# Optimization experiments

Hardware: AMD Instinct MI355X
Metric: run time of the kernel (lower is better)

## Reference

```python
import jax, jax.numpy as jnp
import numpy as np
import math

B, S, D, H = 2, 2048, 2048, 16
HD = D // H  # 128


def _rope(x, cos, sin):
    # x: [b, s, h, hd]; cos/sin: [s, hd//2]
    # torch view_as_complex pairs adjacent elements: (even=real, odd=imag)
    xr = x[..., 0::2]
    xi = x[..., 1::2]
    c = cos[None, :, None, :]
    s = sin[None, :, None, :]
    out_r = xr * c - xi * s
    out_i = xr * s + xi * c
    # interleave back: [..., hd//2, 2] -> [..., hd]
    return jnp.stack([out_r, out_i], axis=-1).reshape(x.shape)


def setup_inputs() -> dict:
    key = jax.random.key(0)
    ks = jax.random.split(key, 5)
    x = jax.random.normal(ks[0], (B, S, D), dtype=jnp.float32)
    std = 1.0 / math.sqrt(D)
    wq = jax.random.normal(ks[1], (D, D), dtype=jnp.float32) * std
    wk = jax.random.normal(ks[2], (D, D), dtype=jnp.float32) * std
    wv = jax.random.normal(ks[3], (D, D), dtype=jnp.float32) * std
    wo = jax.random.normal(ks[4], (D, D), dtype=jnp.float32) * std
    # RoPE frequencies, theta = 10000
    freqs = 1.0 / (10000.0 ** (jnp.arange(0, HD, 2, dtype=jnp.float32) / HD))  # [hd//2]
    t = jnp.arange(S, dtype=jnp.float32)
    angles = jnp.outer(t, freqs)  # [s, hd//2]
    freqs_cos = jnp.cos(angles)
    freqs_sin = jnp.sin(angles)
    # causal additive mask [s, s]
    mask = jnp.triu(jnp.full((S, S), -jnp.inf, dtype=jnp.float32), k=1)
    return {"x": x, "start_pos": 0, "freqs_cos": freqs_cos, "freqs_sin": freqs_sin,
            "mask": mask, "wq": wq, "wk": wk, "wv": wv, "wo": wo}


def reference(x, start_pos, freqs_cos, freqs_sin, mask, wq, wk, wv, wo):
    b, s, d = x.shape
    # projections (torch Linear: y = x @ W.T)
    xq = (x @ wq.T).reshape(b, s, H, HD)
    xk = (x @ wk.T).reshape(b, s, H, HD)
    xv = (x @ wv.T).reshape(b, s, H, HD)
    xq = _rope(xq, freqs_cos, freqs_sin)
    xk = _rope(xk, freqs_cos, freqs_sin)
    # start_pos = 0 prefill: cache[:b, :s] == freshly computed xk/xv
    # scores: [b, h, s_q, s_k]
    scores = jnp.einsum("bqhd,bkhd->bhqk", xq, xk) / math.sqrt(HD)
    scores = scores + mask[None, None, :, :]
    probs = jax.nn.softmax(scores, axis=-1)
    out = jnp.einsum("bhqk,bkhd->bqhd", probs, xv).reshape(b, s, d)
    return out @ wo.T
```

## Files before the change

kernel.cpp:

```cpp
#include <hip/hip_runtime.h>

typedef __attribute__((ext_vector_type(8))) short short8;
typedef __attribute__((ext_vector_type(4))) float f32x4;
typedef __attribute__((ext_vector_type(16))) float f32x16;
typedef unsigned int u32;
typedef __attribute__((ext_vector_type(4))) u32 u32x4;
typedef unsigned short u16;

#define DEV __device__ __forceinline__

DEV void async16(const void* g, void* l) {
  __builtin_amdgcn_global_load_lds((const __attribute__((address_space(1))) u32*)g,
                                   (__attribute__((address_space(3))) u32*)l, 16, 0, 0);
}

DEV u16 f2bf(float f) {
  u32 u = __builtin_bit_cast(u32, f);
  u32 r = (u + 0x7FFFu + ((u >> 16) & 1u)) >> 16;
  return (u16)r;
}
DEV float bf2f(u16 h) { return __builtin_bit_cast(float, (u32)h << 16); }

__global__ void cast_bf16_kernel(const float* __restrict__ in, u16* __restrict__ out, int n4) {
  int stride = gridDim.x * blockDim.x;
  for (int i = blockIdx.x * blockDim.x + threadIdx.x; i < n4; i += stride) {
    float4 v = reinterpret_cast<const float4*>(in)[i];
    ushort4 o = make_ushort4(f2bf(v.x), f2bf(v.y), f2bf(v.z), f2bf(v.w));
    reinterpret_cast<ushort4*>(out)[i] = o;
  }
}

template <int MODE>
__global__ __launch_bounds__(256) void gemm_bt(const u16* __restrict__ A,
                                               const u16* __restrict__ Bw,
                                               void* __restrict__ C) {
  constexpr int K = 2048;
  __shared__ char sm[32768];
  const int tid = threadIdx.x;
  const int lane = tid & 63;
  const int w = tid >> 6;
  const int bx = blockIdx.x & 15;
  const int by = blockIdx.x >> 4;
  const int row0 = by * 128, col0 = bx * 128;
  const int wr = (w >> 1) * 64, wc = (w & 1) * 64;
  f32x4 acc[4][4] = {};

  for (int k0 = 0; k0 < K; k0 += 64) {
    __syncthreads();
#pragma unroll
    for (int i = 0; i < 4; ++i) {
      int slot = tid + i * 256;
      int r = slot >> 3, s = slot & 7;
      int sl = s ^ (r & 7);
      async16(A + (size_t)(row0 + r) * K + (k0 + sl * 8), sm + slot * 16);
    }
#pragma unroll
    for (int i = 0; i < 4; ++i) {
      int slot = tid + i * 256;
      int r = slot >> 3, s = slot & 7;
      int sl = s ^ (r & 7);
      async16(Bw + (size_t)(col0 + r) * K + (k0 + sl * 8), sm + 16384 + slot * 16);
    }
    __syncthreads();
#pragma unroll
    for (int kk = 0; kk < 2; ++kk) {
      short8 af[4], bfr[4];
#pragma unroll
      for (int mi = 0; mi < 4; ++mi) {
        int r = wr + mi * 16 + (lane & 15);
        int ps = (kk * 4 + (lane >> 4)) ^ (r & 7);
        af[mi] = *reinterpret_cast<const short8*>(sm + r * 128 + ps * 16);
      }
#pragma unroll
      for (int ni = 0; ni < 4; ++ni) {
        int r = wc + ni * 16 + (lane & 15);
        int ps = (kk * 4 + (lane >> 4)) ^ (r & 7);
        bfr[ni] = *reinterpret_cast<const short8*>(sm + 16384 + r * 128 + ps * 16);
      }
#pragma unroll
      for (int mi = 0; mi < 4; ++mi)
#pragma unroll
        for (int ni = 0; ni < 4; ++ni)
          acc[mi][ni] = __builtin_amdgcn_mfma_f32_16x16x32_bf16(af[mi], bfr[ni], acc[mi][ni], 0, 0, 0);
    }
  }
#pragma unroll
  for (int mi = 0; mi < 4; ++mi)
#pragma unroll
    for (int ni = 0; ni < 4; ++ni)
#pragma unroll
      for (int r = 0; r < 4; ++r) {
        int gm = row0 + wr + mi * 16 + ((lane >> 4) << 2) + r;
        int gn = col0 + wc + ni * 16 + (lane & 15);
        float v = acc[mi][ni][r];
        if constexpr (MODE == 0) {
          int b = gm >> 11, s = gm & 2047, h = gn >> 7, hd = gn & 127;
          ((u16*)C)[(size_t)((b << 4) | h) * 262144 + (s << 7) + hd] = f2bf(v);
        } else if constexpr (MODE == 2) {
          int b = gm >> 11, s = gm & 2047, h = gn >> 7, hd = gn & 127;
          ((u16*)C)[(size_t)((b << 4) | h) * 262144 + (hd << 11) + s] = f2bf(v);
        } else {
          ((float*)C)[((size_t)gm << 11) + gn] = v;
        }
      }
}

__global__ void rope_kernel(u16* __restrict__ q, u16* __restrict__ k,
                            const float* __restrict__ cb, const float* __restrict__ sb) {
  const float rs = 0.127517436f;
  const int NP = 2 * 16 * 2048 * 64;
  int stride = gridDim.x * blockDim.x;
  for (int i = blockIdx.x * blockDim.x + threadIdx.x; i < 2 * NP; i += stride) {
    int p = (i < NP) ? i : i - NP;
    u16* base = (i < NP) ? q : k;
    float sc = (i < NP) ? rs : 1.0f;
    int fi = p & 63;
    int s = (p >> 6) & 2047;
    u32 v = *reinterpret_cast<u32*>(base + 2 * (size_t)p);
    float xr = bf2f((u16)(v & 0xFFFFu)), xi = bf2f((u16)(v >> 16));
    float c = cb[(s << 6) + fi], sn = sb[(s << 6) + fi];
    float orr = (xr * c - xi * sn) * sc;
    float oi = (xr * sn + xi * c) * sc;
    *reinterpret_cast<u32*>(base + 2 * (size_t)p) = (u32)f2bf(orr) | ((u32)f2bf(oi) << 16);
  }
}

__global__ __launch_bounds__(512, 2) void attn_kernel(const u16* __restrict__ q_ws,
                                                      const u16* __restrict__ k_ws,
                                                      const u16* __restrict__ vt_ws,
                                                      u16* __restrict__ attn_ws) {
  constexpr int S = 2048;
  constexpr float NEGBIG = -3.0e38f;
  __shared__ char sm[65536];
  const int tid = threadIdx.x, lane = tid & 63, w = tid >> 6;
  const int hi = lane >> 5, l31 = lane & 31;
  const int bid = blockIdx.x;
  const int pairA = bid >> 5;
  const int bh = ((bid & 7) << 2) | ((bid >> 3) & 3);
  const int qt = (w < 4) ? pairA : 15 - pairA;
  const int qr0 = qt * 128 + (w & 3) * 32;
  const int ntile = 32 - 2 * pairA;
  const int my_nt = (qr0 >> 6) + 1;

  const u16* qp = q_ws + (size_t)bh * S * 128;
  const u16* kp = k_ws + (size_t)bh * S * 128;
  const u16* vp = vt_ws + (size_t)bh * 128 * S;

  short8 qf[8];
  {
    const u16* qr = qp + (size_t)(qr0 + l31) * 128 + hi * 8;
#pragma unroll
    for (int ks = 0; ks < 8; ++ks) qf[ks] = *reinterpret_cast<const short8*>(qr + ks * 16);
  }
  f32x16 accO[4];
#pragma unroll
  for (int dc = 0; dc < 4; ++dc)
#pragma unroll
    for (int r = 0; r < 16; ++r) accO[dc][r] = 0.f;
  float m = -1e30f, l = 0.f;

  auto stage = [&](int bufoff, int kv0) {
#pragma unroll
    for (int i = 0; i < 2; ++i) {
      int slot = tid + i * 512;
      int r = slot >> 4, s = slot & 15;
      async16(kp + (size_t)(kv0 + r) * 128 + ((s ^ (r & 15)) * 8), sm + bufoff + slot * 16);
    }
#pragma unroll
    for (int i = 0; i < 2; ++i) {
      int slot = tid + i * 512;
      int r = slot >> 3, s = slot & 7;
      async16(vp + (size_t)r * S + kv0 + ((s ^ (r & 7)) * 8), sm + bufoff + 16384 + slot * 16);
    }
  };

  stage(0, 0);
  __syncthreads();

  for (int t = 0; t < ntile; ++t) {
    const char* kb = sm + (t & 1) * 32768;
    const char* vb = kb + 16384;
    if (t + 1 < ntile) stage(((t + 1) & 1) * 32768, (t + 1) * 64);

    if (t < my_nt) {
      f32x16 sacc[2];
#pragma unroll
      for (int jc = 0; jc < 2; ++jc)
#pragma unroll
        for (int r = 0; r < 16; ++r) sacc[jc][r] = 0.f;
      __builtin_amdgcn_s_setprio(1);
#pragma unroll
      for (int jc = 0; jc < 2; ++jc) {
        const char* krp = kb + (jc * 32 + l31) * 256;
        const int sw = l31 & 15;
#pragma unroll
        for (int ks = 0; ks < 8; ++ks) {
          short8 kf = *reinterpret_cast<const short8*>(krp + (((2 * ks + hi) ^ sw) << 4));
          sacc[jc] = __builtin_amdgcn_mfma_f32_32x32x16_bf16(kf, qf[ks], sacc[jc], 0, 0, 0);
        }
      }
      __builtin_amdgcn_s_setprio(0);
      if (t == my_nt - 1) {
#pragma unroll
        for (int jc = 0; jc < 2; ++jc) {
          int thr = qr0 + l31 - t * 64 - 32 * jc - 4 * hi;
#pragma unroll
          for (int r = 0; r < 16; ++r) {
            int c0 = (r & 3) + 8 * (r >> 2);
            if (c0 > thr) sacc[jc][r] = NEGBIG;
          }
        }
      }
      float pmA = NEGBIG, pmB = NEGBIG, pmC = NEGBIG, pmD = NEGBIG;
#pragma unroll
      for (int jc = 0; jc < 2; ++jc)
#pragma unroll
        for (int r = 0; r < 16; r += 4) {
          pmA = fmaxf(pmA, sacc[jc][r]);
          pmB = fmaxf(pmB, sacc[jc][r + 1]);
          pmC = fmaxf(pmC, sacc[jc][r + 2]);
          pmD = fmaxf(pmD, sacc[jc][r + 3]);
        }
      float pmax = fmaxf(fmaxf(pmA, pmB), fmaxf(pmC, pmD));
      pmax = fmaxf(pmax, __shfl_xor(pmax, 32, 64));
      float mnew = fmaxf(m, pmax);
      float scl = exp2f(m - mnew);
      m = mnew;
      float sA = 0.f, sB = 0.f, sC = 0.f, sD = 0.f;
#pragma unroll
      for (int jc = 0; jc < 2; ++jc)
#pragma unroll
        for (int r = 0; r < 16; r += 4) {
          float p0 = exp2f(sacc[jc][r] - mnew);
          float p1 = exp2f(sacc[jc][r + 1] - mnew);
          float p2 = exp2f(sacc[jc][r + 2] - mnew);
          float p3 = exp2f(sacc[jc][r + 3] - mnew);
          sacc[jc][r] = p0; sacc[jc][r + 1] = p1; sacc[jc][r + 2] = p2; sacc[jc][r + 3] = p3;
          sA += p0; sB += p1; sC += p2; sD += p3;
        }
      float ps = (sA + sB) + (sC + sD);
      ps += __shfl_xor(ps, 32, 64);
      l = l * scl + ps;
#pragma unroll
      for (int dc = 0; dc < 4; ++dc)
#pragma unroll
        for (int r = 0; r < 16; ++r) accO[dc][r] *= scl;
      short8 pfrag[4];
#pragma unroll
      for (int ks = 0; ks < 4; ++ks) {
        const int jc = ks >> 1, u8 = (ks & 1) * 8;
        u32 wA = (u32)f2bf(sacc[jc][u8 + 0]) | ((u32)f2bf(sacc[jc][u8 + 1]) << 16);
        u32 wB = (u32)f2bf(sacc[jc][u8 + 2]) | ((u32)f2bf(sacc[jc][u8 + 3]) << 16);
        u32 wC = (u32)f2bf(sacc[jc][u8 + 4]) | ((u32)f2bf(sacc[jc][u8 + 5]) << 16);
        u32 wD = (u32)f2bf(sacc[jc][u8 + 6]) | ((u32)f2bf(sacc[jc][u8 + 7]) << 16);
        u32 qA = __shfl_xor(wA, 32, 64);
        u32 qB = __shfl_xor(wB, 32, 64);
        u32 qC = __shfl_xor(wC, 32, 64);
        u32 qD = __shfl_xor(wD, 32, 64);
        u32x4 t4;
        t4.x = hi ? qC : wA;
        t4.y = hi ? qD : wB;
        t4.z = hi ? wC : qA;
        t4.w = hi ? wD : qB;
        pfrag[ks] = __builtin_bit_cast(short8, t4);
      }
      __builtin_amdgcn_s_setprio(1);
#pragma unroll
      for (int ks = 0; ks < 4; ++ks) {
#pragma unroll
        for (int dc = 0; dc < 4; ++dc) {
          const char* vrp = vb + (dc * 32 + l31) * 128;
          short8 vf = *reinterpret_cast<const short8*>(vrp + (((2 * ks + hi) ^ (l31 & 7)) << 4));
          accO[dc] = __builtin_amdgcn_mfma_f32_32x32x16_bf16(vf, pfrag[ks], accO[dc], 0, 0, 0);
        }
      }
      __builtin_amdgcn_s_setprio(0);
    }
    __syncthreads();
  }

  const int b = bh >> 4, h = bh & 15;
  char* tb = sm + w * 8192;
  float inv = (l > 0.f) ? 1.0f / l : 0.f;
#pragma unroll
  for (int dc = 0; dc < 4; ++dc)
#pragma unroll
    for (int r = 0; r < 16; ++r) {
      int d = dc * 32 + (r & 3) + 8 * (r >> 2) + 4 * hi;
      int byte = l31 * 256 + d * 2;
      *reinterpret_cast<u16*>(tb + (byte ^ ((l31 & 7) << 4))) = f2bf(accO[dc][r] * inv);
    }
  asm volatile("s_waitcnt lgkmcnt(0)" ::: "memory");
#pragma unroll
  for (int i = 0; i < 8; ++i) {
    int r = i * 4 + (lane >> 4);
    int s = lane & 15;
    f32x4 v = *reinterpret_cast<const f32x4*>(tb + r * 256 + ((s ^ (r & 7)) << 4));
    size_t addr = ((size_t)(b * 2048 + qr0 + r) << 11) + (h << 7) + s * 8;
    *reinterpret_cast<f32x4*>(attn_ws + addr) = v;
  }
}

extern "C" void kernel_launch(void* const* d_in, const int* in_sizes, int n_in,
                              void* d_out, int out_size, void* d_ws, size_t ws_size,
                              hipStream_t stream) {
  const float* x = (const float*)d_in[0];
  const float* cb = (const float*)d_in[2];
  const float* sb = (const float*)d_in[3];
  const float* wq = (const float*)d_in[5];
  const float* wk = (const float*)d_in[6];
  const float* wv = (const float*)d_in[7];
  const float* wo = (const float*)d_in[8];

  char* p = (char*)d_ws;
  u16* xb  = (u16*)p; p += (size_t)4096 * 2048 * 2;
  u16* wqb = (u16*)p; p += (size_t)2048 * 2048 * 2;
  u16* wkb = (u16*)p; p += (size_t)2048 * 2048 * 2;
  u16* wvb = (u16*)p; p += (size_t)2048 * 2048 * 2;
  u16* wob = (u16*)p; p += (size_t)2048 * 2048 * 2;
  u16* q_ws = (u16*)p; p += (size_t)4096 * 2048 * 2;
  u16* k_ws = (u16*)p; p += (size_t)4096 * 2048 * 2;
  u16* vt_ws = (u16*)p; p += (size_t)4096 * 2048 * 2;
  u16* attn_ws = xb;

  cast_bf16_kernel<<<2048, 256, 0, stream>>>(x, xb, 4096 * 2048 / 4);
  cast_bf16_kernel<<<1024, 256, 0, stream>>>(wq, wqb, 2048 * 2048 / 4);
  cast_bf16_kernel<<<1024, 256, 0, stream>>>(wk, wkb, 2048 * 2048 / 4);
  cast_bf16_kernel<<<1024, 256, 0, stream>>>(wv, wvb, 2048 * 2048 / 4);
  cast_bf16_kernel<<<1024, 256, 0, stream>>>(wo, wob, 2048 * 2048 / 4);

  gemm_bt<0><<<512, 256, 0, stream>>>(xb, wqb, q_ws);
  gemm_bt<0><<<512, 256, 0, stream>>>(xb, wkb, k_ws);
  gemm_bt<2><<<512, 256, 0, stream>>>(xb, wvb, vt_ws);

  rope_kernel<<<2048, 256, 0, stream>>>(q_ws, k_ws, cb, sb);

  attn_kernel<<<256, 512, 0, stream>>>(q_ws, k_ws, vt_ws, attn_ws);

  gemm_bt<3><<<512, 256, 0, stream>>>(attn_ws, wob, d_out);
}
```

Before: 297.1 us.

## Fuse casts and QKV GEMMs, split attention blocks, add lazy softmax rescale

```diff
diff --git a/kernel.cpp b/kernel.cpp
--- a/kernel.cpp
+++ b/kernel.cpp
@@ -21,10 +21,30 @@
 }
 DEV float bf2f(u16 h) { return __builtin_bit_cast(float, (u32)h << 16); }
 
-__global__ void cast_bf16_kernel(const float* __restrict__ in, u16* __restrict__ out, int n4) {
+DEV u32 cvtpk(float lo, float hi) {
+  u32 r;
+  asm("v_cvt_pk_bf16_f32 %0, %1, %2" : "=v"(r) : "v"(lo), "v"(hi));
+  return r;
+}
+
+__global__ void cast_all_kernel(const float* __restrict__ x, const float* __restrict__ wq,
+                                const float* __restrict__ wk, const float* __restrict__ wv,
+                                const float* __restrict__ wo, u16* __restrict__ out) {
+  constexpr int XN = 2097152;
+  constexpr int WN = 1048576;
+  constexpr int TOT = XN + 4 * WN;
   int stride = gridDim.x * blockDim.x;
-  for (int i = blockIdx.x * blockDim.x + threadIdx.x; i < n4; i += stride) {
-    float4 v = reinterpret_cast<const float4*>(in)[i];
+  for (int i = blockIdx.x * blockDim.x + threadIdx.x; i < TOT; i += stride) {
+    const float* src;
+    int off;
+    if (i < XN) {
+      src = x; off = i;
+    } else {
+      int j = i - XN, wsel = j >> 20;
+      const float* ws4[4] = {wq, wk, wv, wo};
+      src = ws4[wsel]; off = j & (WN - 1);
+    }
+    float4 v = reinterpret_cast<const float4*>(src)[off];
     ushort4 o = make_ushort4(f2bf(v.x), f2bf(v.y), f2bf(v.z), f2bf(v.w));
     reinterpret_cast<ushort4*>(out)[i] = o;
   }
@@ -33,14 +53,16 @@
 template <int MODE>
 __global__ __launch_bounds__(256) void gemm_bt(const u16* __restrict__ A,
                                                const u16* __restrict__ Bw,
-                                               void* __restrict__ C) {
+                                               void* __restrict__ C0,
+                                               u16* __restrict__ C1,
+                                               u16* __restrict__ C2) {
   constexpr int K = 2048;
   __shared__ char sm[32768];
   const int tid = threadIdx.x;
   const int lane = tid & 63;
   const int w = tid >> 6;
-  const int bx = blockIdx.x & 15;
-  const int by = blockIdx.x >> 4;
+  const int by = blockIdx.x & 31;
+  const int bx = blockIdx.x >> 5;
   const int row0 = by * 128, col0 = bx * 128;
   const int wr = (w >> 1) * 64, wc = (w & 1) * 64;
   f32x4 acc[4][4] = {};
@@ -93,14 +115,16 @@
         int gm = row0 + wr + mi * 16 + ((lane >> 4) << 2) + r;
         int gn = col0 + wc + ni * 16 + (lane & 15);
         float v = acc[mi][ni][r];
-        if constexpr (MODE == 0) {
-          int b = gm >> 11, s = gm & 2047, h = gn >> 7, hd = gn & 127;
-          ((u16*)C)[(size_t)((b << 4) | h) * 262144 + (s << 7) + hd] = f2bf(v);
-        } else if constexpr (MODE == 2) {
-          int b = gm >> 11, s = gm & 2047, h = gn >> 7, hd = gn & 127;
-          ((u16*)C)[(size_t)((b << 4) | h) * 262144 + (hd << 11) + s] = f2bf(v);
+        if constexpr (MODE == 4) {
+          int tsel = gn >> 11, nn = gn & 2047;
+          int b = gm >> 11, s = gm & 2047, h = nn >> 7, hd = nn & 127;
+          u16* dst = (tsel == 0) ? (u16*)C0 : (tsel == 1) ? C1 : C2;
+          if (tsel < 2)
+            dst[(size_t)((b << 4) | h) * 262144 + (s << 7) + hd] = f2bf(v);
+          else
+            dst[(size_t)((b << 4) | h) * 262144 + (hd << 11) + s] = f2bf(v);
         } else {
-          ((float*)C)[((size_t)gm << 11) + gn] = v;
+          ((float*)C0)[((size_t)gm << 11) + gn] = v;
         }
       }
 }
@@ -125,7 +149,7 @@
   }
 }
 
-__global__ __launch_bounds__(512, 2) void attn_kernel(const u16* __restrict__ q_ws,
+__global__ __launch_bounds__(256, 2) void attn_kernel(const u16* __restrict__ q_ws,
                                                       const u16* __restrict__ k_ws,
                                                       const u16* __restrict__ vt_ws,
                                                       u16* __restrict__ attn_ws) {
@@ -135,11 +159,11 @@
   const int tid = threadIdx.x, lane = tid & 63, w = tid >> 6;
   const int hi = lane >> 5, l31 = lane & 31;
   const int bid = blockIdx.x;
-  const int pairA = bid >> 5;
+  const int qtr = bid >> 5;
+  const int qt = (qtr < 8) ? qtr : 23 - qtr;
   const int bh = ((bid & 7) << 2) | ((bid >> 3) & 3);
-  const int qt = (w < 4) ? pairA : 15 - pairA;
-  const int qr0 = qt * 128 + (w & 3) * 32;
-  const int ntile = 32 - 2 * pairA;
+  const int qr0 = qt * 128 + w * 32;
+  const int ntile = 2 * qt + 2;
   const int my_nt = (qr0 >> 6) + 1;
 
   const u16* qp = q_ws + (size_t)bh * S * 128;
@@ -161,14 +185,14 @@
 
   auto stage = [&](int bufoff, int kv0) {
 #pragma unroll
-    for (int i = 0; i < 2; ++i) {
-      int slot = tid + i * 512;
+    for (int i = 0; i < 4; ++i) {
+      int slot = tid + i * 256;
       int r = slot >> 4, s = slot & 15;
       async16(kp + (size_t)(kv0 + r) * 128 + ((s ^ (r & 15)) * 8), sm + bufoff + slot * 16);
     }
 #pragma unroll
-    for (int i = 0; i < 2; ++i) {
-      int slot = tid + i * 512;
+    for (int i = 0; i < 4; ++i) {
+      int slot = tid + i * 256;
       int r = slot >> 3, s = slot & 7;
       async16(vp + (size_t)r * S + kv0 + ((s ^ (r & 7)) * 8), sm + bufoff + 16384 + slot * 16);
     }
@@ -223,36 +247,39 @@
         }
       float pmax = fmaxf(fmaxf(pmA, pmB), fmaxf(pmC, pmD));
       pmax = fmaxf(pmax, __shfl_xor(pmax, 32, 64));
-      float mnew = fmaxf(m, pmax);
-      float scl = exp2f(m - mnew);
-      m = mnew;
+      if (!__all(pmax - m <= 8.0f)) {
+        float mnew = fmaxf(m, pmax);
+        float scl = exp2f(m - mnew);
+        m = mnew;
+        l *= scl;
+#pragma unroll
+        for (int dc = 0; dc < 4; ++dc)
+#pragma unroll
+          for (int r = 0; r < 16; ++r) accO[dc][r] *= scl;
+      }
       float sA = 0.f, sB = 0.f, sC = 0.f, sD = 0.f;
 #pragma unroll
       for (int jc = 0; jc < 2; ++jc)
 #pragma unroll
         for (int r = 0; r < 16; r += 4) {
-          float p0 = exp2f(sacc[jc][r] - mnew);
-          float p1 = exp2f(sacc[jc][r + 1] - mnew);
-          float p2 = exp2f(sacc[jc][r + 2] - mnew);
-          float p3 = exp2f(sacc[jc][r + 3] - mnew);
+          float p0 = exp2f(sacc[jc][r] - m);
+          float p1 = exp2f(sacc[jc][r + 1] - m);
+          float p2 = exp2f(sacc[jc][r + 2] - m);
+          float p3 = exp2f(sacc[jc][r + 3] - m);
           sacc[jc][r] = p0; sacc[jc][r + 1] = p1; sacc[jc][r + 2] = p2; sacc[jc][r + 3] = p3;
           sA += p0; sB += p1; sC += p2; sD += p3;
         }
       float ps = (sA + sB) + (sC + sD);
       ps += __shfl_xor(ps, 32, 64);
-      l = l * scl + ps;
-#pragma unroll
-      for (int dc = 0; dc < 4; ++dc)
-#pragma unroll
-        for (int r = 0; r < 16; ++r) accO[dc][r] *= scl;
+      l += ps;
       short8 pfrag[4];
 #pragma unroll
       for (int ks = 0; ks < 4; ++ks) {
         const int jc = ks >> 1, u8 = (ks & 1) * 8;
-        u32 wA = (u32)f2bf(sacc[jc][u8 + 0]) | ((u32)f2bf(sacc[jc][u8 + 1]) << 16);
-        u32 wB = (u32)f2bf(sacc[jc][u8 + 2]) | ((u32)f2bf(sacc[jc][u8 + 3]) << 16);
-        u32 wC = (u32)f2bf(sacc[jc][u8 + 4]) | ((u32)f2bf(sacc[jc][u8 + 5]) << 16);
-        u32 wD = (u32)f2bf(sacc[jc][u8 + 6]) | ((u32)f2bf(sacc[jc][u8 + 7]) << 16);
+        u32 wA = cvtpk(sacc[jc][u8 + 0], sacc[jc][u8 + 1]);
+        u32 wB = cvtpk(sacc[jc][u8 + 2], sacc[jc][u8 + 3]);
+        u32 wC = cvtpk(sacc[jc][u8 + 4], sacc[jc][u8 + 5]);
+        u32 wD = cvtpk(sacc[jc][u8 + 6], sacc[jc][u8 + 7]);
         u32 qA = __shfl_xor(wA, 32, 64);
         u32 qB = __shfl_xor(wB, 32, 64);
         u32 qC = __shfl_xor(wC, 32, 64);
@@ -322,20 +349,15 @@
   u16* k_ws = (u16*)p; p += (size_t)4096 * 2048 * 2;
   u16* vt_ws = (u16*)p; p += (size_t)4096 * 2048 * 2;
   u16* attn_ws = xb;
-
-  cast_bf16_kernel<<<2048, 256, 0, stream>>>(x, xb, 4096 * 2048 / 4);
-  cast_bf16_kernel<<<1024, 256, 0, stream>>>(wq, wqb, 2048 * 2048 / 4);
-  cast_bf16_kernel<<<1024, 256, 0, stream>>>(wk, wkb, 2048 * 2048 / 4);
-  cast_bf16_kernel<<<1024, 256, 0, stream>>>(wv, wvb, 2048 * 2048 / 4);
-  cast_bf16_kernel<<<1024, 256, 0, stream>>>(wo, wob, 2048 * 2048 / 4);
-
-  gemm_bt<0><<<512, 256, 0, stream>>>(xb, wqb, q_ws);
-  gemm_bt<0><<<512, 256, 0, stream>>>(xb, wkb, k_ws);
-  gemm_bt<2><<<512, 256, 0, stream>>>(xb, wvb, vt_ws);
+  (void)wkb; (void)wvb;
+
+  cast_all_kernel<<<3072, 256, 0, stream>>>(x, wq, wk, wv, wo, xb);
+
+  gemm_bt<4><<<1536, 256, 0, stream>>>(xb, wqb, q_ws, k_ws, vt_ws);
 
   rope_kernel<<<2048, 256, 0, stream>>>(q_ws, k_ws, cb, sb);
 
-  attn_kernel<<<256, 512, 0, stream>>>(q_ws, k_ws, vt_ws, attn_ws);
-
-  gemm_bt<3><<<512, 256, 0, stream>>>(attn_ws, wob, d_out);
-}
+  attn_kernel<<<512, 256, 0, stream>>>(q_ws, k_ws, vt_ws, attn_ws);
+
+  gemm_bt<3><<<512, 256, 0, stream>>>(attn_ws, wob, d_out, nullptr, nullptr);
+}
```

Measured after the change: 271.8 us. 8.5% less time.
